# Optimization experiments

Measured on AMD Instinct MI355X. Metric: run time of the kernel, lower is better.

## Reference

```python
import jax, jax.numpy as jnp
import numpy as np
import math

B, S, C = 4, 2048, 128
H, DK, DV, K = 8, 64, 64, 3


def setup_inputs() -> dict:
    key = jax.random.key(0)
    ks = jax.random.split(key, 12)
    sd = 0.05
    return {
        "x": jax.random.normal(ks[0], (B, S, C), dtype=jnp.float32),
        "length": jax.random.randint(ks[1], (B,), 1, S + 1, dtype=jnp.int32),
        "wq": jax.random.normal(ks[2], (H * DK, C, K), dtype=jnp.float32) * sd,
        "bq": jnp.zeros((H * DK,), dtype=jnp.float32),
        "wk": jax.random.normal(ks[3], (H * DK, C, K), dtype=jnp.float32) * sd,
        "bk": jnp.zeros((H * DK,), dtype=jnp.float32),
        "wv": jax.random.normal(ks[4], (H * DV, C), dtype=jnp.float32) * sd,
        "bv": jnp.zeros((H * DV,), dtype=jnp.float32),
        "w1": jax.random.normal(ks[5], (DV, H * DV), dtype=jnp.float32) * sd,
        "b1": jnp.zeros((DV,), dtype=jnp.float32),
        "w2": jax.random.normal(ks[6], (1, DV), dtype=jnp.float32) * sd,
        "b2": jnp.zeros((1,), dtype=jnp.float32),
    }


def _causal_conv(x, w, b):
    # x: (b,s,c), w: (o,c,k) torch Conv1d layout -> (b,s,o), causal (left) padding
    y = jax.lax.conv_general_dilated(
        x.transpose(0, 2, 1), w, window_strides=(1,), padding=[(K - 1, 0)],
        dimension_numbers=("NCH", "OIH", "NCH"))
    return y.transpose(0, 2, 1) + b


def _split_heads(x, d):
    b, s, _ = x.shape
    return x.reshape(b, s, H, d).transpose(0, 2, 1, 3)  # (b,h,s,d)


def reference(x, length, wq, bq, wk, bk, wv, bv, w1, b1, w2, b2):
    q = _split_heads(_causal_conv(x, wq, bq), DK)            # (b,h,s,dk)
    k = _split_heads(_causal_conv(x, wk, bk), DK)            # (b,h,s,dk)
    v = _split_heads(jax.nn.relu(x @ wv.T + bv), DV)         # (b,h,s,dv)

    attn = jnp.einsum("bhqd,bhkd->bhqk", q, k) / math.sqrt(DK)
    # future mask: additive -1e9 above the diagonal (matches triu * -1e9 + softmax)
    future = jnp.triu(jnp.ones((S, S), dtype=attn.dtype), k=1) * (-1e9)
    score = jax.nn.softmax(attn + future, axis=-1)
    # padding mask: zero query rows >= length[b]
    row_valid = (jnp.arange(S)[None, :] < length[:, None]).astype(score.dtype)
    score = score * row_valid[:, None, :, None]              # (b,h,s,s)

    out1 = jnp.einsum("bhqk,bhkd->bhqd", score, v)           # (b,h,s,dv)
    out2 = out1.transpose(0, 2, 1, 3).reshape(x.shape[0], S, H * DV)
    out3 = jax.nn.relu(out2 @ w1.T + b1) @ w2.T + b2         # (b,s,1)
    return out3, score
```

## Files before the change

kernel.cpp:

```cpp
#include <hip/hip_runtime.h>

#define S_ 2048
#define C_ 128
#define B_ 4
#define H_ 8
#define D_ 64

typedef __attribute__((ext_vector_type(8))) short bf16x8;
typedef __attribute__((ext_vector_type(4))) float f32x4;

__device__ inline unsigned short f2bf(float f) {
    union { float f; unsigned int u; } c; c.f = f;
    unsigned int u = c.u;
    unsigned int r = (u + 0x7FFFu + ((u >> 16) & 1u)) >> 16;
    return (unsigned short)r;
}
__device__ inline float bf2f(unsigned short s) {
    union { unsigned int u; float f; } c; c.u = ((unsigned int)s) << 16;
    return c.f;
}

__global__ __launch_bounds__(256) void prep_kernel(
    const float* __restrict__ x,
    const float* __restrict__ wq, const float* __restrict__ wk,
    const float* __restrict__ wv, const float* __restrict__ w1,
    unsigned short* __restrict__ xh,
    unsigned short* __restrict__ wPackQ, unsigned short* __restrict__ wPackK,
    unsigned short* __restrict__ wPackV, float* __restrict__ w1T)
{
    int idx = blockIdx.x * 256 + threadIdx.x;
    if (idx < 1048576) {
        xh[idx] = f2bf(x[idx]);
    } else if (idx < 1245184) {
        int i = idx - 1048576;
        int t = i >> 16, r = i & 65535;
        int o = r >> 7, c = r & 127;
        wPackQ[i] = f2bf(wq[o * 384 + c * 3 + t]);
    } else if (idx < 1441792) {
        int i = idx - 1245184;
        int t = i >> 16, r = i & 65535;
        int o = r >> 7, c = r & 127;
        wPackK[i] = f2bf(wk[o * 384 + c * 3 + t]);
    } else if (idx < 1507328) {
        int i = idx - 1441792;
        wPackV[i] = f2bf(wv[i]);
    } else if (idx < 1540096) {
        int i = idx - 1507328;
        int j = i >> 6, d = i & 63;
        w1T[i] = w1[d * 512 + j];
    }
}

__global__ __launch_bounds__(256) void qkv_kernel(
    const unsigned short* __restrict__ xh,
    const unsigned short* __restrict__ wPackQ, const unsigned short* __restrict__ wPackK,
    const unsigned short* __restrict__ wPackV,
    const float* __restrict__ bq, const float* __restrict__ bk,
    const float* __restrict__ bv,
    unsigned short* __restrict__ Qh, unsigned short* __restrict__ Kh,
    unsigned short* __restrict__ VhT)
{
    __shared__ __align__(16) short xs[130 * 136];
    __shared__ __align__(16) short ws[64 * 136];

    int s0 = blockIdx.x * 128;
    int ns = blockIdx.y;
    int b = blockIdx.z;
    int sectype = ns >> 3;
    int h = ns & 7;
    int bh = b * H_ + h;
    int tid = threadIdx.x;
    int w = tid >> 6;
    int lane = tid & 63;
    int col = lane & 15;
    int quad = lane >> 4;

    for (int i = tid; i < 2080; i += 256) {
        int row = i >> 4, c8 = (i & 15) << 3;
        int s = s0 - 2 + row;
        uint4 v = {0u, 0u, 0u, 0u};
        if (s >= 0) v = *(const uint4*)&xh[((long)b * S_ + s) * C_ + c8];
        *(uint4*)&xs[row * 136 + c8] = v;
    }

    f32x4 acc[2][4];
    #pragma unroll
    for (int rt = 0; rt < 2; rt++)
        #pragma unroll
        for (int nt = 0; nt < 4; nt++) acc[rt][nt] = (f32x4){0.f, 0.f, 0.f, 0.f};

    int tlo = (sectype == 2) ? 2 : 0;
    int thi = 3;
    const unsigned short* wsel =
        (sectype == 0) ? wPackQ : (sectype == 1) ? wPackK : wPackV;

    bool first = true;
    for (int t = tlo; t < thi; t++) {
        if (!first) __syncthreads();
        {
            long wbase = (sectype == 2) ? ((long)h * 64 * 128)
                                        : ((long)t * 65536 + (long)h * 64 * 128);
            for (int i = tid; i < 1024; i += 256) {
                int row = i >> 4, c8 = (i & 15) << 3;
                *(uint4*)&ws[row * 136 + c8] = *(const uint4*)&wsel[wbase + row * 128 + c8];
            }
        }
        __syncthreads();
        first = false;

        #pragma unroll
        for (int kc = 0; kc < 4; kc++) {
            int ko = kc * 32 + quad * 8;
            bf16x8 a0 = *(const bf16x8*)&xs[(w * 32 + col + t) * 136 + ko];
            bf16x8 a1 = *(const bf16x8*)&xs[(w * 32 + 16 + col + t) * 136 + ko];
            #pragma unroll
            for (int nt = 0; nt < 4; nt++) {
                bf16x8 bfr = *(const bf16x8*)&ws[(nt * 16 + col) * 136 + ko];
                acc[0][nt] = __builtin_amdgcn_mfma_f32_16x16x32_bf16(a0, bfr, acc[0][nt], 0, 0, 0);
                acc[1][nt] = __builtin_amdgcn_mfma_f32_16x16x32_bf16(a1, bfr, acc[1][nt], 0, 0, 0);
            }
        }
    }

    if (sectype == 0) {
        #pragma unroll
        for (int nt = 0; nt < 4; nt++) {
            float bias = bq[h * 64 + nt * 16 + col];
            #pragma unroll
            for (int rt = 0; rt < 2; rt++)
                #pragma unroll
                for (int r = 0; r < 4; r++) {
                    int s = s0 + w * 32 + rt * 16 + quad * 4 + r;
                    Qh[((long)bh * S_ + s) * D_ + nt * 16 + col] =
                        f2bf((acc[rt][nt][r] + bias) * 0.125f);
                }
        }
    } else if (sectype == 1) {
        #pragma unroll
        for (int nt = 0; nt < 4; nt++) {
            float bias = bk[h * 64 + nt * 16 + col];
            #pragma unroll
            for (int rt = 0; rt < 2; rt++)
                #pragma unroll
                for (int r = 0; r < 4; r++) {
                    int s = s0 + w * 32 + rt * 16 + quad * 4 + r;
                    Kh[((long)bh * S_ + s) * D_ + nt * 16 + col] =
                        f2bf(acc[rt][nt][r] + bias);
                }
        }
    } else {
        __syncthreads();
        #pragma unroll
        for (int nt = 0; nt < 4; nt++) {
            float bias = bv[h * 64 + nt * 16 + col];
            #pragma unroll
            for (int rt = 0; rt < 2; rt++)
                #pragma unroll
                for (int r = 0; r < 4; r++) {
                    int sl = w * 32 + rt * 16 + quad * 4 + r;
                    ws[(nt * 16 + col) * 136 + sl] =
                        (short)f2bf(fmaxf(acc[rt][nt][r] + bias, 0.f));
                }
        }
        __syncthreads();
        for (int i = tid; i < 1024; i += 256) {
            int row = i >> 4, c8 = (i & 15) << 3;
            *(uint4*)&VhT[((long)bh * D_ + row) * S_ + s0 + c8] =
                *(const uint4*)&ws[row * 136 + c8];
        }
    }
}

__global__ __launch_bounds__(256) void attn_kernel(
    const unsigned short* __restrict__ Qh, const unsigned short* __restrict__ Kh,
    const unsigned short* __restrict__ VhT, const int* __restrict__ length,
    float* __restrict__ score, float* __restrict__ out2)
{
    __shared__ __align__(16) short QVs[64 * 72];
    __shared__ __align__(16) short Ks[64 * 72];
    __shared__ __align__(16) short Pfh[64 * 72];

    int idx = blockIdx.x;
    int xcd = idx & 7;
    int slot = idx >> 3;
    int bh = xcd * 4 + (slot & 3);
    int qt = 31 - (slot >> 2);
    int b = bh >> 3, h = bh & 7;
    int q0 = qt * 64;
    int tid = threadIdx.x;
    int w = tid >> 6;
    int lane = tid & 63;
    int col = lane & 15;
    int quad = lane >> 4;
    int len = length[b];

    const unsigned short* Qb = Qh + (long)bh * S_ * D_;
    const unsigned short* Kb = Kh + (long)bh * S_ * D_;
    const unsigned short* Vtb = VhT + (long)bh * D_ * S_;
    float* scb = score + (long)bh * S_ * S_;

    {
        int r = tid >> 2, c16 = (tid & 3) * 16;
        *(uint4*)&QVs[r * 72 + c16] = *(const uint4*)&Qb[(q0 + r) * D_ + c16];
        *(uint4*)&QVs[r * 72 + c16 + 8] = *(const uint4*)&Qb[(q0 + r) * D_ + c16 + 8];
    }
    __syncthreads();
    int arow = w * 16 + col;
    bf16x8 aq0 = *(const bf16x8*)&QVs[arow * 72 + quad * 8];
    bf16x8 aq1 = *(const bf16x8*)&QVs[arow * 72 + 32 + quad * 8];

    float lrun[4];
    #pragma unroll
    for (int r = 0; r < 4; r++) lrun[r] = 0.f;

    for (int kt = 0; kt <= qt; kt++) {
        __syncthreads();
        {
            int r = tid >> 2, c16 = (tid & 3) * 16;
            *(uint4*)&Ks[r * 72 + c16] = *(const uint4*)&Kb[(kt * 64 + r) * D_ + c16];
            *(uint4*)&Ks[r * 72 + c16 + 8] = *(const uint4*)&Kb[(kt * 64 + r) * D_ + c16 + 8];
        }
        __syncthreads();

        f32x4 acc[4];
        #pragma unroll
        for (int n = 0; n < 4; n++) acc[n] = (f32x4){0.f, 0.f, 0.f, 0.f};
        #pragma unroll
        for (int n = 0; n < 4; n++) {
            bf16x8 b0 = *(const bf16x8*)&Ks[(n * 16 + col) * 72 + quad * 8];
            acc[n] = __builtin_amdgcn_mfma_f32_16x16x32_bf16(aq0, b0, acc[n], 0, 0, 0);
            bf16x8 b1 = *(const bf16x8*)&Ks[(n * 16 + col) * 72 + 32 + quad * 8];
            acc[n] = __builtin_amdgcn_mfma_f32_16x16x32_bf16(aq1, b1, acc[n], 0, 0, 0);
        }
        if (kt == qt) {
            #pragma unroll
            for (int n = 0; n < 4; n++) {
                int kk = kt * 64 + n * 16 + col;
                #pragma unroll
                for (int r = 0; r < 4; r++) {
                    int q = q0 + w * 16 + quad * 4 + r;
                    if (kk > q) acc[n][r] = -1.0e30f;
                }
            }
        }
        #pragma unroll
        for (int r = 0; r < 4; r++) {
            lrun[r] += __expf(acc[0][r]) + __expf(acc[1][r]) +
                       __expf(acc[2][r]) + __expf(acc[3][r]);
        }
    }

    #pragma unroll
    for (int off = 1; off < 16; off <<= 1) {
        #pragma unroll
        for (int r = 0; r < 4; r++) lrun[r] += __shfl_xor(lrun[r], off, 64);
    }
    float linv[4];
    #pragma unroll
    for (int r = 0; r < 4; r++) linv[r] = 1.0f / lrun[r];

    f32x4 oacc[4];
    #pragma unroll
    for (int n = 0; n < 4; n++) oacc[n] = (f32x4){0.f, 0.f, 0.f, 0.f};

    for (int kt = 0; kt <= qt; kt++) {
        __syncthreads();
        {
            int r = tid >> 2, c16 = (tid & 3) * 16;
            *(uint4*)&Ks[r * 72 + c16] = *(const uint4*)&Kb[(kt * 64 + r) * D_ + c16];
            *(uint4*)&Ks[r * 72 + c16 + 8] = *(const uint4*)&Kb[(kt * 64 + r) * D_ + c16 + 8];
            *(uint4*)&QVs[r * 72 + c16] = *(const uint4*)&Vtb[r * S_ + kt * 64 + c16];
            *(uint4*)&QVs[r * 72 + c16 + 8] = *(const uint4*)&Vtb[r * S_ + kt * 64 + c16 + 8];
        }
        __syncthreads();

        f32x4 acc[4];
        #pragma unroll
        for (int n = 0; n < 4; n++) acc[n] = (f32x4){0.f, 0.f, 0.f, 0.f};
        #pragma unroll
        for (int n = 0; n < 4; n++) {
            bf16x8 b0 = *(const bf16x8*)&Ks[(n * 16 + col) * 72 + quad * 8];
            acc[n] = __builtin_amdgcn_mfma_f32_16x16x32_bf16(aq0, b0, acc[n], 0, 0, 0);
            bf16x8 b1 = *(const bf16x8*)&Ks[(n * 16 + col) * 72 + 32 + quad * 8];
            acc[n] = __builtin_amdgcn_mfma_f32_16x16x32_bf16(aq1, b1, acc[n], 0, 0, 0);
        }

        bool diag = (kt == qt);
        #pragma unroll
        for (int n = 0; n < 4; n++) {
            int kk = kt * 64 + n * 16 + col;
            #pragma unroll
            for (int r = 0; r < 4; r++) {
                int q = q0 + w * 16 + quad * 4 + r;
                float p = __expf(acc[n][r]) * linv[r];
                if (q >= len || (diag && kk > q)) p = 0.f;
                Pfh[(w * 16 + quad * 4 + r) * 72 + n * 16 + col] = (short)f2bf(p);
            }
        }
        bf16x8 pa0 = *(const bf16x8*)&Pfh[(w * 16 + col) * 72 + quad * 8];
        bf16x8 pa1 = *(const bf16x8*)&Pfh[(w * 16 + col) * 72 + 32 + quad * 8];
        #pragma unroll
        for (int n = 0; n < 4; n++) {
            bf16x8 v0 = *(const bf16x8*)&QVs[(n * 16 + col) * 72 + quad * 8];
            oacc[n] = __builtin_amdgcn_mfma_f32_16x16x32_bf16(pa0, v0, oacc[n], 0, 0, 0);
            bf16x8 v1 = *(const bf16x8*)&QVs[(n * 16 + col) * 72 + 32 + quad * 8];
            oacc[n] = __builtin_amdgcn_mfma_f32_16x16x32_bf16(pa1, v1, oacc[n], 0, 0, 0);
        }

        __syncthreads();
        #pragma unroll
        for (int i = 0; i < 4; i++) {
            int idx2 = tid + i * 256;
            int row = idx2 >> 4, k0 = (idx2 & 15) * 4;
            uint2 pk = *(const uint2*)&Pfh[row * 72 + k0];
            f32x4 v;
            v[0] = bf2f((unsigned short)(pk.x & 0xFFFFu));
            v[1] = bf2f((unsigned short)(pk.x >> 16));
            v[2] = bf2f((unsigned short)(pk.y & 0xFFFFu));
            v[3] = bf2f((unsigned short)(pk.y >> 16));
            __builtin_nontemporal_store(v,
                (f32x4*)&scb[(long)(q0 + row) * S_ + kt * 64 + k0]);
        }
    }

    #pragma unroll
    for (int n = 0; n < 4; n++) {
        #pragma unroll
        for (int r = 0; r < 4; r++) {
            int q = q0 + w * 16 + quad * 4 + r;
            out2[((long)(b * S_ + q)) * 512 + h * 64 + n * 16 + col] = oacc[n][r];
        }
    }

    f32x4 z = (f32x4){0.f, 0.f, 0.f, 0.f};
    for (int kt2 = qt + 1; kt2 < 32; kt2++) {
        #pragma unroll
        for (int it = 0; it < 4; it++) {
            int idx2 = tid + it * 256;
            int rr = idx2 >> 4, cc = idx2 & 15;
            __builtin_nontemporal_store(z,
                (f32x4*)&scb[(long)(q0 + rr) * S_ + kt2 * 64 + cc * 4]);
        }
    }
}

__global__ __launch_bounds__(256) void mlp_kernel(
    const float* __restrict__ out2, const float* __restrict__ w1T,
    const float* __restrict__ b1, const float* __restrict__ w2,
    const float* __restrict__ b2, float* __restrict__ out3)
{
    __shared__ float xr[2048];
    int sg0 = blockIdx.x * 4;
    int tid = threadIdx.x;
    for (int i = tid; i < 2048; i += 256) xr[i] = out2[(long)sg0 * 512 + i];
    __syncthreads();

    int sl = tid >> 6, d = tid & 63;
    float acc = 0.f;
    const float* xp = &xr[sl * 512];
    #pragma unroll 8
    for (int j = 0; j < 512; j++) acc += xp[j] * w1T[j * 64 + d];
    float hval = fmaxf(acc + b1[d], 0.f);
    float p = hval * w2[d];
    #pragma unroll
    for (int off = 32; off > 0; off >>= 1) p += __shfl_xor(p, off, 64);
    if (d == 0) out3[sg0 + sl] = p + b2[0];
}

extern "C" void kernel_launch(void* const* d_in, const int* in_sizes, int n_in,
                              void* d_out, int out_size, void* d_ws, size_t ws_size,
                              hipStream_t stream) {
    const float* x      = (const float*)d_in[0];
    const int*   length = (const int*)  d_in[1];
    const float* wq     = (const float*)d_in[2];
    const float* bq     = (const float*)d_in[3];
    const float* wk     = (const float*)d_in[4];
    const float* bk     = (const float*)d_in[5];
    const float* wv     = (const float*)d_in[6];
    const float* bv     = (const float*)d_in[7];
    const float* w1     = (const float*)d_in[8];
    const float* b1     = (const float*)d_in[9];
    const float* w2     = (const float*)d_in[10];
    const float* b2     = (const float*)d_in[11];

    float* out3  = (float*)d_out;
    float* score = (float*)d_out + 8192;

    float* ws  = (float*)d_ws;
    unsigned short* xh     = (unsigned short*)ws;  ws += 524288;
    unsigned short* wPackQ = (unsigned short*)ws;  ws += 98304;
    unsigned short* wPackK = (unsigned short*)ws;  ws += 98304;
    unsigned short* wPackV = (unsigned short*)ws;  ws += 32768;
    float* w1T = ws;  ws += 32768;
    unsigned short* Qh  = (unsigned short*)ws;  ws += 2097152;
    unsigned short* Kh  = (unsigned short*)ws;  ws += 2097152;
    unsigned short* VhT = (unsigned short*)ws;  ws += 2097152;
    float* o2  = ws;  ws += 4194304;

    hipLaunchKernelGGL(prep_kernel, dim3(6016), dim3(256), 0, stream,
                       x, wq, wk, wv, w1, xh, wPackQ, wPackK, wPackV, w1T);
    hipLaunchKernelGGL(qkv_kernel, dim3(16, 24, 4), dim3(256), 0, stream,
                       xh, wPackQ, wPackK, wPackV, bq, bk, bv, Qh, Kh, VhT);
    hipLaunchKernelGGL(attn_kernel, dim3(1024), dim3(256), 0, stream,
                       Qh, Kh, VhT, length, score, o2);
    hipLaunchKernelGGL(mlp_kernel, dim3(2048), dim3(256), 0, stream,
                       o2, w1T, b1, w2, b2, out3);
}
```

Baseline: 666.1 us.

## Merge QKV sections per block, double-buffer K in stats pass, per-warp score stores

The QKV kernel now computes Q, K and V in a single block that loads the x tile once, instead of three separate block types, which cuts the grid to a third. In the attention kernel the first (row-sum) pass double-buffers K tiles so the next tile's load overlaps the current compute. The score write-back is changed so each warp stores only the rows it produced, which removes a block-wide barrier per tile, and the P buffer stride is padded to 76. Query tiles are also reordered to interleave heavy and light tiles. The trade-off is less parallelism in the QKV kernel, plus more shared memory and a longer serial chain per block.

```diff
diff --git a/kernel.cpp b/kernel.cpp
--- a/kernel.cpp
+++ b/kernel.cpp
@@ -64,10 +64,8 @@
     __shared__ __align__(16) short ws[64 * 136];
 
     int s0 = blockIdx.x * 128;
-    int ns = blockIdx.y;
+    int h = blockIdx.y;
     int b = blockIdx.z;
-    int sectype = ns >> 3;
-    int h = ns & 7;
     int bh = b * H_ + h;
     int tid = threadIdx.x;
     int w = tid >> 6;
@@ -83,90 +81,86 @@
         *(uint4*)&xs[row * 136 + c8] = v;
     }
 
-    f32x4 acc[2][4];
-    #pragma unroll
-    for (int rt = 0; rt < 2; rt++)
-        #pragma unroll
-        for (int nt = 0; nt < 4; nt++) acc[rt][nt] = (f32x4){0.f, 0.f, 0.f, 0.f};
-
-    int tlo = (sectype == 2) ? 2 : 0;
-    int thi = 3;
-    const unsigned short* wsel =
-        (sectype == 0) ? wPackQ : (sectype == 1) ? wPackK : wPackV;
-
-    bool first = true;
-    for (int t = tlo; t < thi; t++) {
-        if (!first) __syncthreads();
-        {
-            long wbase = (sectype == 2) ? ((long)h * 64 * 128)
-                                        : ((long)t * 65536 + (long)h * 64 * 128);
+    for (int sec = 0; sec < 3; sec++) {
+        const unsigned short* wsel = (sec == 0) ? wPackQ : (sec == 1) ? wPackK : wPackV;
+        int tlo = (sec == 2) ? 2 : 0;
+
+        f32x4 acc[2][4];
+        #pragma unroll
+        for (int rt = 0; rt < 2; rt++)
+            #pragma unroll
+            for (int nt = 0; nt < 4; nt++) acc[rt][nt] = (f32x4){0.f, 0.f, 0.f, 0.f};
+
+        for (int t = tlo; t < 3; t++) {
+            if (!(sec == 0 && t == 0)) __syncthreads();
+            long wbase = (sec == 2) ? ((long)h * 8192)
+                                    : ((long)t * 65536 + (long)h * 8192);
             for (int i = tid; i < 1024; i += 256) {
                 int row = i >> 4, c8 = (i & 15) << 3;
                 *(uint4*)&ws[row * 136 + c8] = *(const uint4*)&wsel[wbase + row * 128 + c8];
             }
-        }
-        __syncthreads();
-        first = false;
-
-        #pragma unroll
-        for (int kc = 0; kc < 4; kc++) {
-            int ko = kc * 32 + quad * 8;
-            bf16x8 a0 = *(const bf16x8*)&xs[(w * 32 + col + t) * 136 + ko];
-            bf16x8 a1 = *(const bf16x8*)&xs[(w * 32 + 16 + col + t) * 136 + ko];
+            __syncthreads();
+
+            #pragma unroll
+            for (int kc = 0; kc < 4; kc++) {
+                int ko = kc * 32 + quad * 8;
+                bf16x8 a0 = *(const bf16x8*)&xs[(w * 32 + col + t) * 136 + ko];
+                bf16x8 a1 = *(const bf16x8*)&xs[(w * 32 + 16 + col + t) * 136 + ko];
+                #pragma unroll
+                for (int nt = 0; nt < 4; nt++) {
+                    bf16x8 bfr = *(const bf16x8*)&ws[(nt * 16 + col) * 136 + ko];
+                    acc[0][nt] = __builtin_amdgcn_mfma_f32_16x16x32_bf16(a0, bfr, acc[0][nt], 0, 0, 0);
+                    acc[1][nt] = __builtin_amdgcn_mfma_f32_16x16x32_bf16(a1, bfr, acc[1][nt], 0, 0, 0);
+                }
+            }
+        }
+
+        if (sec == 0) {
             #pragma unroll
             for (int nt = 0; nt < 4; nt++) {
-                bf16x8 bfr = *(const bf16x8*)&ws[(nt * 16 + col) * 136 + ko];
-                acc[0][nt] = __builtin_amdgcn_mfma_f32_16x16x32_bf16(a0, bfr, acc[0][nt], 0, 0, 0);
-                acc[1][nt] = __builtin_amdgcn_mfma_f32_16x16x32_bf16(a1, bfr, acc[1][nt], 0, 0, 0);
-            }
-        }
-    }
-
-    if (sectype == 0) {
-        #pragma unroll
-        for (int nt = 0; nt < 4; nt++) {
-            float bias = bq[h * 64 + nt * 16 + col];
-            #pragma unroll
-            for (int rt = 0; rt < 2; rt++)
+                float bias = bq[h * 64 + nt * 16 + col];
                 #pragma unroll
-                for (int r = 0; r < 4; r++) {
-                    int s = s0 + w * 32 + rt * 16 + quad * 4 + r;
-                    Qh[((long)bh * S_ + s) * D_ + nt * 16 + col] =
-                        f2bf((acc[rt][nt][r] + bias) * 0.125f);
-                }
-        }
-    } else if (sectype == 1) {
-        #pragma unroll
-        for (int nt = 0; nt < 4; nt++) {
-            float bias = bk[h * 64 + nt * 16 + col];
-            #pragma unroll
-            for (int rt = 0; rt < 2; rt++)
+                for (int rt = 0; rt < 2; rt++)
+                    #pragma unroll
+                    for (int r = 0; r < 4; r++) {
+                        int s = s0 + w * 32 + rt * 16 + quad * 4 + r;
+                        Qh[((long)bh * S_ + s) * D_ + nt * 16 + col] =
+                            f2bf((acc[rt][nt][r] + bias) * 0.125f);
+                    }
+            }
+        } else if (sec == 1) {
+            #pragma unroll
+            for (int nt = 0; nt < 4; nt++) {
+                float bias = bk[h * 64 + nt * 16 + col];
                 #pragma unroll
-                for (int r = 0; r < 4; r++) {
-                    int s = s0 + w * 32 + rt * 16 + quad * 4 + r;
-                    Kh[((long)bh * S_ + s) * D_ + nt * 16 + col] =
-                        f2bf(acc[rt][nt][r] + bias);
-                }
-        }
-    } else {
-        __syncthreads();
-        #pragma unroll
-        for (int nt = 0; nt < 4; nt++) {
-            float bias = bv[h * 64 + nt * 16 + col];
-            #pragma unroll
-            for (int rt = 0; rt < 2; rt++)
+                for (int rt = 0; rt < 2; rt++)
+                    #pragma unroll
+                    for (int r = 0; r < 4; r++) {
+                        int s = s0 + w * 32 + rt * 16 + quad * 4 + r;
+                        Kh[((long)bh * S_ + s) * D_ + nt * 16 + col] =
+                            f2bf(acc[rt][nt][r] + bias);
+                    }
+            }
+        } else {
+            __syncthreads();
+            #pragma unroll
+            for (int nt = 0; nt < 4; nt++) {
+                float bias = bv[h * 64 + nt * 16 + col];
                 #pragma unroll
-                for (int r = 0; r < 4; r++) {
-                    int sl = w * 32 + rt * 16 + quad * 4 + r;
-                    ws[(nt * 16 + col) * 136 + sl] =
-                        (short)f2bf(fmaxf(acc[rt][nt][r] + bias, 0.f));
-                }
-        }
-        __syncthreads();
-        for (int i = tid; i < 1024; i += 256) {
-            int row = i >> 4, c8 = (i & 15) << 3;
-            *(uint4*)&VhT[((long)bh * D_ + row) * S_ + s0 + c8] =
-                *(const uint4*)&ws[row * 136 + c8];
+                for (int rt = 0; rt < 2; rt++)
+                    #pragma unroll
+                    for (int r = 0; r < 4; r++) {
+                        int sl = w * 32 + rt * 16 + quad * 4 + r;
+                        ws[(nt * 16 + col) * 136 + sl] =
+                            (short)f2bf(fmaxf(acc[rt][nt][r] + bias, 0.f));
+                    }
+            }
+            __syncthreads();
+            for (int i = tid; i < 1024; i += 256) {
+                int row = i >> 4, c8 = (i & 15) << 3;
+                *(uint4*)&VhT[((long)bh * D_ + row) * S_ + s0 + c8] =
+                    *(const uint4*)&ws[row * 136 + c8];
+            }
         }
     }
 }
@@ -176,15 +170,15 @@
     const unsigned short* __restrict__ VhT, const int* __restrict__ length,
     float* __restrict__ score, float* __restrict__ out2)
 {
-    __shared__ __align__(16) short QVs[64 * 72];
-    __shared__ __align__(16) short Ks[64 * 72];
-    __shared__ __align__(16) short Pfh[64 * 72];
+    __shared__ __align__(16) short Kbuf[2][64 * 72];
+    __shared__ __align__(16) short Pfh[64 * 76];
 
     int idx = blockIdx.x;
     int xcd = idx & 7;
     int slot = idx >> 3;
+    int t = slot >> 2;
+    int qt = (t < 16) ? t : 47 - t;
     int bh = xcd * 4 + (slot & 3);
-    int qt = 31 - (slot >> 2);
     int b = bh >> 3, h = bh & 7;
     int q0 = qt * 64;
     int tid = threadIdx.x;
@@ -199,37 +193,44 @@
     const unsigned short* Vtb = VhT + (long)bh * D_ * S_;
     float* scb = score + (long)bh * S_ * S_;
 
+    int srow_ = tid >> 2, sc16_ = (tid & 3) * 16;
+
     {
-        int r = tid >> 2, c16 = (tid & 3) * 16;
-        *(uint4*)&QVs[r * 72 + c16] = *(const uint4*)&Qb[(q0 + r) * D_ + c16];
-        *(uint4*)&QVs[r * 72 + c16 + 8] = *(const uint4*)&Qb[(q0 + r) * D_ + c16 + 8];
+        *(uint4*)&Pfh[srow_ * 76 + sc16_]     = *(const uint4*)&Qb[(q0 + srow_) * D_ + sc16_];
+        *(uint4*)&Pfh[srow_ * 76 + sc16_ + 8] = *(const uint4*)&Qb[(q0 + srow_) * D_ + sc16_ + 8];
     }
     __syncthreads();
     int arow = w * 16 + col;
-    bf16x8 aq0 = *(const bf16x8*)&QVs[arow * 72 + quad * 8];
-    bf16x8 aq1 = *(const bf16x8*)&QVs[arow * 72 + 32 + quad * 8];
+    bf16x8 aq0 = *(const bf16x8*)&Pfh[arow * 76 + quad * 8];
+    bf16x8 aq1 = *(const bf16x8*)&Pfh[arow * 76 + 32 + quad * 8];
 
     float lrun[4];
     #pragma unroll
     for (int r = 0; r < 4; r++) lrun[r] = 0.f;
 
+    {
+        *(uint4*)&Kbuf[0][srow_ * 72 + sc16_]     = *(const uint4*)&Kb[srow_ * D_ + sc16_];
+        *(uint4*)&Kbuf[0][srow_ * 72 + sc16_ + 8] = *(const uint4*)&Kb[srow_ * D_ + sc16_ + 8];
+    }
+    __syncthreads();
+
     for (int kt = 0; kt <= qt; kt++) {
-        __syncthreads();
-        {
-            int r = tid >> 2, c16 = (tid & 3) * 16;
-            *(uint4*)&Ks[r * 72 + c16] = *(const uint4*)&Kb[(kt * 64 + r) * D_ + c16];
-            *(uint4*)&Ks[r * 72 + c16 + 8] = *(const uint4*)&Kb[(kt * 64 + r) * D_ + c16 + 8];
-        }
-        __syncthreads();
+        int buf = kt & 1;
+        if (kt < qt) {
+            *(uint4*)&Kbuf[1 - buf][srow_ * 72 + sc16_] =
+                *(const uint4*)&Kb[((kt + 1) * 64 + srow_) * D_ + sc16_];
+            *(uint4*)&Kbuf[1 - buf][srow_ * 72 + sc16_ + 8] =
+                *(const uint4*)&Kb[((kt + 1) * 64 + srow_) * D_ + sc16_ + 8];
+        }
 
         f32x4 acc[4];
         #pragma unroll
         for (int n = 0; n < 4; n++) acc[n] = (f32x4){0.f, 0.f, 0.f, 0.f};
         #pragma unroll
         for (int n = 0; n < 4; n++) {
-            bf16x8 b0 = *(const bf16x8*)&Ks[(n * 16 + col) * 72 + quad * 8];
+            bf16x8 b0 = *(const bf16x8*)&Kbuf[buf][(n * 16 + col) * 72 + quad * 8];
             acc[n] = __builtin_amdgcn_mfma_f32_16x16x32_bf16(aq0, b0, acc[n], 0, 0, 0);
-            bf16x8 b1 = *(const bf16x8*)&Ks[(n * 16 + col) * 72 + 32 + quad * 8];
+            bf16x8 b1 = *(const bf16x8*)&Kbuf[buf][(n * 16 + col) * 72 + 32 + quad * 8];
             acc[n] = __builtin_amdgcn_mfma_f32_16x16x32_bf16(aq1, b1, acc[n], 0, 0, 0);
         }
         if (kt == qt) {
@@ -248,6 +249,7 @@
             lrun[r] += __expf(acc[0][r]) + __expf(acc[1][r]) +
                        __expf(acc[2][r]) + __expf(acc[3][r]);
         }
+        __syncthreads();
     }
 
     #pragma unroll
@@ -266,11 +268,14 @@
     for (int kt = 0; kt <= qt; kt++) {
         __syncthreads();
         {
-            int r = tid >> 2, c16 = (tid & 3) * 16;
-            *(uint4*)&Ks[r * 72 + c16] = *(const uint4*)&Kb[(kt * 64 + r) * D_ + c16];
-            *(uint4*)&Ks[r * 72 + c16 + 8] = *(const uint4*)&Kb[(kt * 64 + r) * D_ + c16 + 8];
-            *(uint4*)&QVs[r * 72 + c16] = *(const uint4*)&Vtb[r * S_ + kt * 64 + c16];
-            *(uint4*)&QVs[r * 72 + c16 + 8] = *(const uint4*)&Vtb[r * S_ + kt * 64 + c16 + 8];
+            *(uint4*)&Kbuf[0][srow_ * 72 + sc16_] =
+                *(const uint4*)&Kb[(kt * 64 + srow_) * D_ + sc16_];
+            *(uint4*)&Kbuf[0][srow_ * 72 + sc16_ + 8] =
+                *(const uint4*)&Kb[(kt * 64 + srow_) * D_ + sc16_ + 8];
+            *(uint4*)&Kbuf[1][srow_ * 72 + sc16_] =
+                *(const uint4*)&Vtb[srow_ * S_ + kt * 64 + sc16_];
+            *(uint4*)&Kbuf[1][srow_ * 72 + sc16_ + 8] =
+                *(const uint4*)&Vtb[srow_ * S_ + kt * 64 + sc16_ + 8];
         }
         __syncthreads();
 
@@ -279,9 +284,9 @@
         for (int n = 0; n < 4; n++) acc[n] = (f32x4){0.f, 0.f, 0.f, 0.f};
         #pragma unroll
         for (int n = 0; n < 4; n++) {
-            bf16x8 b0 = *(const bf16x8*)&Ks[(n * 16 + col) * 72 + quad * 8];
+            bf16x8 b0 = *(const bf16x8*)&Kbuf[0][(n * 16 + col) * 72 + quad * 8];
             acc[n] = __builtin_amdgcn_mfma_f32_16x16x32_bf16(aq0, b0, acc[n], 0, 0, 0);
-            bf16x8 b1 = *(const bf16x8*)&Ks[(n * 16 + col) * 72 + 32 + quad * 8];
+            bf16x8 b1 = *(const bf16x8*)&Kbuf[0][(n * 16 + col) * 72 + 32 + quad * 8];
             acc[n] = __builtin_amdgcn_mfma_f32_16x16x32_bf16(aq1, b1, acc[n], 0, 0, 0);
         }
 
@@ -294,32 +299,33 @@
                 int q = q0 + w * 16 + quad * 4 + r;
                 float p = __expf(acc[n][r]) * linv[r];
                 if (q >= len || (diag && kk > q)) p = 0.f;
-                Pfh[(w * 16 + quad * 4 + r) * 72 + n * 16 + col] = (short)f2bf(p);
-            }
-        }
-        bf16x8 pa0 = *(const bf16x8*)&Pfh[(w * 16 + col) * 72 + quad * 8];
-        bf16x8 pa1 = *(const bf16x8*)&Pfh[(w * 16 + col) * 72 + 32 + quad * 8];
+                Pfh[(w * 16 + quad * 4 + r) * 76 + n * 16 + col] = (short)f2bf(p);
+            }
+        }
+        bf16x8 pa0 = *(const bf16x8*)&Pfh[(w * 16 + col) * 76 + quad * 8];
+        bf16x8 pa1 = *(const bf16x8*)&Pfh[(w * 16 + col) * 76 + 32 + quad * 8];
         #pragma unroll
         for (int n = 0; n < 4; n++) {
-            bf16x8 v0 = *(const bf16x8*)&QVs[(n * 16 + col) * 72 + quad * 8];
+            bf16x8 v0 = *(const bf16x8*)&Kbuf[1][(n * 16 + col) * 72 + quad * 8];
             oacc[n] = __builtin_amdgcn_mfma_f32_16x16x32_bf16(pa0, v0, oacc[n], 0, 0, 0);
-            bf16x8 v1 = *(const bf16x8*)&QVs[(n * 16 + col) * 72 + 32 + quad * 8];
+            bf16x8 v1 = *(const bf16x8*)&Kbuf[1][(n * 16 + col) * 72 + 32 + quad * 8];
             oacc[n] = __builtin_amdgcn_mfma_f32_16x16x32_bf16(pa1, v1, oacc[n], 0, 0, 0);
         }
 
-        __syncthreads();
-        #pragma unroll
-        for (int i = 0; i < 4; i++) {
-            int idx2 = tid + i * 256;
-            int row = idx2 >> 4, k0 = (idx2 & 15) * 4;
-            uint2 pk = *(const uint2*)&Pfh[row * 72 + k0];
-            f32x4 v;
-            v[0] = bf2f((unsigned short)(pk.x & 0xFFFFu));
-            v[1] = bf2f((unsigned short)(pk.x >> 16));
-            v[2] = bf2f((unsigned short)(pk.y & 0xFFFFu));
-            v[3] = bf2f((unsigned short)(pk.y >> 16));
-            __builtin_nontemporal_store(v,
-                (f32x4*)&scb[(long)(q0 + row) * S_ + kt * 64 + k0]);
+        {
+            int row = w * 16 + (lane >> 2);
+            int c16 = (lane & 3) * 16;
+            #pragma unroll
+            for (int j = 0; j < 4; j++) {
+                uint2 pk = *(const uint2*)&Pfh[row * 76 + c16 + j * 4];
+                f32x4 v;
+                v[0] = bf2f((unsigned short)(pk.x & 0xFFFFu));
+                v[1] = bf2f((unsigned short)(pk.x >> 16));
+                v[2] = bf2f((unsigned short)(pk.y & 0xFFFFu));
+                v[3] = bf2f((unsigned short)(pk.y >> 16));
+                __builtin_nontemporal_store(v,
+                    (f32x4*)&scb[(long)(q0 + row) * S_ + kt * 64 + c16 + j * 4]);
+            }
         }
     }
 
@@ -399,7 +405,7 @@
 
     hipLaunchKernelGGL(prep_kernel, dim3(6016), dim3(256), 0, stream,
                        x, wq, wk, wv, w1, xh, wPackQ, wPackK, wPackV, w1T);
-    hipLaunchKernelGGL(qkv_kernel, dim3(16, 24, 4), dim3(256), 0, stream,
+    hipLaunchKernelGGL(qkv_kernel, dim3(16, 8, 4), dim3(256), 0, stream,
                        xh, wPackQ, wPackK, wPackV, bq, bk, bv, Qh, Kh, VhT);
     hipLaunchKernelGGL(attn_kernel, dim3(1024), dim3(256), 0, stream,
                        Qh, Kh, VhT, length, score, o2);
```

After: 1.173 ms. +76.1%, slower.
